# Kernel tuning notes

Hardware: AMD Instinct MI355X
Metric: run time of the kernel (lower is better)

## Reference

```python
import jax, jax.numpy as jnp
import numpy as np

QMAX = 255.0  # bit=8 unsigned activation range


def ste_round(x):
    # straight-through round: exact integer rounding in fwd, identity grad
    return x + jax.lax.stop_gradient(jnp.round(x) - x)


def conv3x3(x, w, stride=1):
    return jax.lax.conv_general_dilated(
        x, w, window_strides=(stride, stride), padding=((1, 1), (1, 1)),
        dimension_numbers=('NCHW', 'OIHW', 'NCHW'))


def setup_inputs() -> dict:
    key = jax.random.key(0)
    k0, k1, k2 = jax.random.split(key, 3)
    N, C, H, W = 64, 256, 28, 28
    # uint8 activations and int8 (symmetric) weights, stored as integer-valued fp32
    x = jax.random.randint(k0, (N, C, H, W), 0, 256).astype(jnp.float32)
    w1 = jax.random.randint(k1, (C, C, 3, 3), -128, 128).astype(jnp.float32)
    w2 = jax.random.randint(k2, (C, C, 3, 3), -128, 128).astype(jnp.float32)
    f = jnp.float32
    return dict(
        x=x, w1=w1, w2=w2,
        s_x=f(0.05), z_x=f(128.0),
        s_w1=f(0.01), s_conv1=f(0.08), z_conv1=f(120.0),
        s_w2=f(0.01), s_conv2=f(0.07), z_conv2=f(130.0),
        s_add=f(0.09), z_add=f(125.0))


def qconv(x_q, w_q, s_in, z_in, s_w, s_out, z_out, stride=1):
    # integer-arithmetic conv: sum((x - z_in) * w) then requantize
    acc = conv3x3(x_q - z_in, w_q, stride)
    M = s_in * s_w / s_out  # per-cluster requant multiplier (cluster 0)
    return jnp.clip(ste_round(M * acc) + z_out, 0.0, QMAX)


def qadd(a, s_a, z_a, b, s_b, z_b, s_out, z_out):
    # fused dequant of both branches + residual add + requant
    y = (s_a / s_out) * (a - z_a) + (s_b / s_out) * (b - z_b)
    return jnp.clip(ste_round(y) + z_out, 0.0, QMAX)


def reference(x, w1, w2, s_x, z_x, s_w1, s_conv1, z_conv1,
              s_w2, s_conv2, z_conv2, s_add, z_add):
    out = qconv(x, w1, s_x, z_x, s_w1, s_conv1, z_conv1)          # conv1
    out = qconv(out, w2, s_conv1, z_conv1, s_w2, s_conv2, z_conv2)  # conv2
    return qadd(x, s_x, z_x, out, s_conv2, z_conv2, s_add, z_add)   # shortcut
```

## Files before the change

kernel.cpp:

```cpp
#include <hip/hip_runtime.h>
#include <stdint.h>

#define HWP 784
#define NPOS 50176

typedef int int4v  __attribute__((ext_vector_type(4)));
typedef int int16v __attribute__((ext_vector_type(16)));
using as1_cv = const __attribute__((address_space(1))) void;
using as3_v  = __attribute__((address_space(3))) void;

__global__ __launch_bounds__(256) void k_x_to_nhwc(const float* __restrict__ x,
                                                   int8_t* __restrict__ x8) {
    __shared__ __align__(16) int8_t tile[64][116];
    int b = blockIdx.x;
    int ct = b & 3;
    int hwt = (b >> 2) % 7;
    int n = b / 28;
    int c0 = ct * 64, hw0 = hwt * 112;
    int tid = threadIdx.x;
#pragma unroll
    for (int k = 0; k < 28; ++k) {
        int e = tid + k * 256;
        int c = e / 112, hh = e % 112;
        float v = x[((size_t)(n * 256 + c0 + c)) * HWP + hw0 + hh];
        tile[c][hh] = (int8_t)((int)v - 128);
    }
    __syncthreads();
    int cc = tid & 63;
    int pb = tid >> 6;
#pragma unroll
    for (int j = 0; j < 28; ++j) {
        int pi = pb + j * 4;
        x8[((size_t)(n * HWP + hw0 + pi)) * 256 + c0 + cc] = tile[cc][pi];
    }
}

__global__ __launch_bounds__(256) void k_w_prep(const float* __restrict__ w,
                                                int8_t* __restrict__ w8,
                                                int* __restrict__ wsum) {
    __shared__ int red[256];
    const int oc = blockIdx.x;
    const int t = threadIdx.x;
    const float* src = w + (size_t)oc * 2304 + (size_t)t * 9;
    const int g = oc >> 5;
    const int l = ((t >> 4) & 1) * 32 + (oc & 31);
    const int j = t & 15;
    const int s2 = (t >> 5) & 1;
    const int kb = t >> 6;
    int acc = 0;
#pragma unroll
    for (int tap = 0; tap < 9; ++tap) {
        int wv = (int)src[tap];
        acc += wv;
        int oo = ((((tap * 4 + kb) * 2 + s2) * 8 + g) * 64 + l) * 16 + j;
        w8[oo] = (int8_t)wv;
    }
    red[t] = acc;
    __syncthreads();
    for (int st = 128; st > 0; st >>= 1) {
        if (t < st) red[t] += red[t + st];
        __syncthreads();
    }
    if (t == 0) wsum[oc] = red[0];
}

__global__ __launch_bounds__(256) void k_qconv(const int8_t* __restrict__ in8,
        const int8_t* __restrict__ w8, const int* __restrict__ wsum,
        const float* __restrict__ s_in_p, const float* __restrict__ s_w_p,
        const float* __restrict__ s_out_p, const float* __restrict__ z_in_p,
        const float* __restrict__ z_out_p, int8_t* __restrict__ out8) {
    __shared__ __align__(16) int8_t slab[32768];
    const int tid = threadIdx.x;
    const int lane = tid & 63;
    const int half = lane >> 5;
    const int wv = tid >> 6;
    const int p0 = blockIdx.x * 64;

    {
        const int base_byte = (p0 - 29) * 256;
        const int maxb = NPOS * 256 - 16;
#pragma unroll
        for (int i = 0; i < 8; ++i) {
            int chunkid = tid + i * 256;
            int q = chunkid >> 4;
            int cslot = chunkid & 15;
            int gchunk = cslot ^ (q & 15);
            int src = base_byte + q * 256 + gchunk * 16;
            src = src < 0 ? 0 : (src > maxb ? maxb : src);
            __builtin_amdgcn_global_load_lds((as1_cv*)(in8 + src),
                                             (as3_v*)&slab[chunkid * 16], 16, 0, 0);
        }
    }

    int rowpos[2], ph[2], pw[2];
#pragma unroll
    for (int mt = 0; mt < 2; ++mt) {
        rowpos[mt] = mt * 32 + (lane & 31);
        int p = p0 + rowpos[mt];
        int hw = p % HWP;
        ph[mt] = hw / 28;
        pw[mt] = hw % 28;
    }

    const int zi = (int)z_in_p[0] - 128;
    const int spl = (zi & 0xff) * 0x01010101;
    int4v pad;
    pad[0] = spl; pad[1] = spl; pad[2] = spl; pad[3] = spl;

    int16v acc[2][2];
#pragma unroll
    for (int mt = 0; mt < 2; ++mt)
#pragma unroll
        for (int nt = 0; nt < 2; ++nt)
#pragma unroll
            for (int r = 0; r < 16; ++r) acc[mt][nt][r] = 0;

    const int8_t* wlane = w8 + ((size_t)(wv * 2 * 64 + lane)) * 16;

    __syncthreads();

#pragma unroll 1
    for (int kb = 0; kb < 4; ++kb) {
#pragma unroll
        for (int tap = 0; tap < 9; ++tap) {
            const int dh = tap / 3 - 1;
            const int dw = tap % 3 - 1;
            const int8_t* wb = wlane + (size_t)(tap * 4 + kb) * 16384;
            int4v b0[2], b1[2];
#pragma unroll
            for (int nt = 0; nt < 2; ++nt) {
                b0[nt] = *(const int4v*)(wb + nt * 1024);
                b1[nt] = *(const int4v*)(wb + 8192 + nt * 1024);
            }
            int4v a0[2], a1[2];
#pragma unroll
            for (int mt = 0; mt < 2; ++mt) {
                int q = rowpos[mt] + dh * 28 + dw + 29;
                int sw = q & 15;
                int base = q * 256;
                int4v v0 = *(const int4v*)&slab[base + ((kb * 4 + half) ^ sw) * 16];
                int4v v1 = *(const int4v*)&slab[base + ((kb * 4 + 2 + half) ^ sw) * 16];
                bool ok = ((unsigned)(ph[mt] + dh) < 28u) & ((unsigned)(pw[mt] + dw) < 28u);
                a0[mt] = ok ? v0 : pad;
                a1[mt] = ok ? v1 : pad;
            }
#pragma unroll
            for (int mt = 0; mt < 2; ++mt)
#pragma unroll
                for (int nt = 0; nt < 2; ++nt) {
                    acc[mt][nt] = __builtin_amdgcn_mfma_i32_32x32x32_i8(a0[mt], b0[nt], acc[mt][nt], 0, 0, 0);
                    acc[mt][nt] = __builtin_amdgcn_mfma_i32_32x32x32_i8(a1[mt], b1[nt], acc[mt][nt], 0, 0, 0);
                }
        }
    }

    const float Mf = s_in_p[0] * s_w_p[0] / s_out_p[0];
    const float zof = z_out_p[0];
    const int zoffi = 128 - (int)z_in_p[0];
#pragma unroll
    for (int nt = 0; nt < 2; ++nt) {
        int oc = wv * 64 + nt * 32 + (lane & 31);
        int corr = zoffi * wsum[oc];
#pragma unroll
        for (int mt = 0; mt < 2; ++mt) {
#pragma unroll
            for (int r = 0; r < 16; ++r) {
                int row = (r & 3) + 8 * (r >> 2) + 4 * half;
                int pos = p0 + mt * 32 + row;
                float q = rintf(Mf * (float)(acc[mt][nt][r] + corr)) + zof;
                q = fminf(fmaxf(q, 0.0f), 255.0f);
                out8[(size_t)pos * 256 + oc] = (int8_t)((int)q - 128);
            }
        }
    }
}

__global__ __launch_bounds__(256) void k_final(const int8_t* __restrict__ x8,
        const int8_t* __restrict__ o2,
        const float* __restrict__ sxp, const float* __restrict__ zxp,
        const float* __restrict__ s2p, const float* __restrict__ z2p,
        const float* __restrict__ sap, const float* __restrict__ zap,
        float* __restrict__ out) {
    __shared__ __align__(16) int8_t ta[128 * 260 + 16];
    __shared__ __align__(16) int8_t tb[128 * 260 + 16];
    const int tid = threadIdx.x;
    const int p0 = blockIdx.x * 128;
    const uint32_t* xa = (const uint32_t*)(x8 + (size_t)p0 * 256);
    const uint32_t* xb = (const uint32_t*)(o2 + (size_t)p0 * 256);
    uint32_t* la = (uint32_t*)ta;
    uint32_t* lb = (uint32_t*)tb;
#pragma unroll
    for (int k = 0; k < 32; ++k) {
        int d = tid + k * 256;
        int idx = (d >> 6) * 65 + (d & 63);
        la[idx] = xa[d];
        lb[idx] = xb[d];
    }
    __syncthreads();
    const float ra = sxp[0] / sap[0];
    const float rb = s2p[0] / sap[0];
    const float zx = zxp[0];
    const float z2 = z2p[0];
    const float za = zap[0];
#pragma unroll 4
    for (int it = 0; it < 128; ++it) {
        int idx = tid + it * 256;
        int oc = idx >> 7;
        int pp = idx & 127;
        float av = (float)((int)ta[pp * 260 + oc] + 128) - zx;
        float bv = (float)((int)tb[pp * 260 + oc] + 128) - z2;
        float y = ra * av + rb * bv;
        float q = rintf(y) + za;
        q = fminf(fmaxf(q, 0.0f), 255.0f);
        int pz = p0 + pp;
        int n = pz / HWP, hh = pz % HWP;
        out[((size_t)(n * 256 + oc)) * HWP + hh] = q;
    }
}

extern "C" void kernel_launch(void* const* d_in, const int* in_sizes, int n_in,
                              void* d_out, int out_size, void* d_ws, size_t ws_size,
                              hipStream_t stream) {
    (void)in_sizes; (void)n_in; (void)out_size; (void)ws_size;
    const float* x    = (const float*)d_in[0];
    const float* w1   = (const float*)d_in[1];
    const float* w2   = (const float*)d_in[2];
    const float* s_x  = (const float*)d_in[3];
    const float* z_x  = (const float*)d_in[4];
    const float* s_w1 = (const float*)d_in[5];
    const float* s_c1 = (const float*)d_in[6];
    const float* z_c1 = (const float*)d_in[7];
    const float* s_w2 = (const float*)d_in[8];
    const float* s_c2 = (const float*)d_in[9];
    const float* z_c2 = (const float*)d_in[10];
    const float* s_ad = (const float*)d_in[11];
    const float* z_ad = (const float*)d_in[12];
    float* out = (float*)d_out;

    int8_t* ws   = (int8_t*)d_ws;
    int8_t* x8   = ws;
    int8_t* o1   = ws + 12845056;
    int8_t* o2   = ws + 25690112;
    int8_t* w8a  = ws + 38535168;
    int8_t* w8b  = ws + 39124992;
    int*    wsum1 = (int*)(ws + 39714816);
    int*    wsum2 = (int*)(ws + 39715840);

    k_x_to_nhwc<<<1792, 256, 0, stream>>>(x, x8);
    k_w_prep<<<256, 256, 0, stream>>>(w1, w8a, wsum1);
    k_w_prep<<<256, 256, 0, stream>>>(w2, w8b, wsum2);
    k_qconv<<<784, 256, 0, stream>>>(x8, w8a, wsum1, s_x, s_w1, s_c1, z_x, z_c1, o1);
    k_qconv<<<784, 256, 0, stream>>>(o1, w8b, wsum2, s_c1, s_w2, s_c2, z_c1, z_c2, o2);
    k_final<<<392, 256, 0, stream>>>(x8, o2, s_x, z_x, s_c2, z_c2, s_ad, z_ad, out);
}
```

Before: 225.5 us.

## Fuse residual add into conv2 and retile conv over positions and channel groups

The conv kernel now gives each block 256 positions and one 64-channel output group (grid 196x4) rather than 64 positions and all channels, so the input slab (now 80KB of LDS) is reused by every wave. Weight fragments are register double-buffered one step ahead, and the loop is reordered tap-outer so boundary masks are computed once per tap. The second conv is templated to fuse the quantized residual add and the NCHW float store, removing the separate final kernel and the o2 round trip through memory. In exchange, the larger LDS footprint reduces occupancy, and each input slab is loaded four times, once per channel-group block.

```diff
diff --git a/kernel.cpp b/kernel.cpp
--- a/kernel.cpp
+++ b/kernel.cpp
@@ -64,23 +64,28 @@
     if (t == 0) wsum[oc] = red[0];
 }
 
-__global__ __launch_bounds__(256) void k_qconv(const int8_t* __restrict__ in8,
+template<bool FUSED>
+__global__ __launch_bounds__(256) void k_qconv_t(const int8_t* __restrict__ in8,
         const int8_t* __restrict__ w8, const int* __restrict__ wsum,
         const float* __restrict__ s_in_p, const float* __restrict__ s_w_p,
         const float* __restrict__ s_out_p, const float* __restrict__ z_in_p,
-        const float* __restrict__ z_out_p, int8_t* __restrict__ out8) {
-    __shared__ __align__(16) int8_t slab[32768];
+        const float* __restrict__ z_out_p, int8_t* __restrict__ out8,
+        const int8_t* __restrict__ x8, const float* __restrict__ sxp,
+        const float* __restrict__ zxp, const float* __restrict__ sap,
+        const float* __restrict__ zap, float* __restrict__ outf) {
+    __shared__ __align__(16) int8_t slab[81920];
     const int tid = threadIdx.x;
     const int lane = tid & 63;
     const int half = lane >> 5;
     const int wv = tid >> 6;
-    const int p0 = blockIdx.x * 64;
+    const int p0 = blockIdx.x * 256;
+    const int g = blockIdx.y;
 
     {
         const int base_byte = (p0 - 29) * 256;
         const int maxb = NPOS * 256 - 16;
 #pragma unroll
-        for (int i = 0; i < 8; ++i) {
+        for (int i = 0; i < 20; ++i) {
             int chunkid = tid + i * 256;
             int q = chunkid >> 4;
             int cslot = chunkid & 15;
@@ -95,7 +100,7 @@
     int rowpos[2], ph[2], pw[2];
 #pragma unroll
     for (int mt = 0; mt < 2; ++mt) {
-        rowpos[mt] = mt * 32 + (lane & 31);
+        rowpos[mt] = wv * 64 + mt * 32 + (lane & 31);
         int p = p0 + rowpos[mt];
         int hw = p % HWP;
         ph[mt] = hw / 28;
@@ -115,106 +120,120 @@
 #pragma unroll
             for (int r = 0; r < 16; ++r) acc[mt][nt][r] = 0;
 
-    const int8_t* wlane = w8 + ((size_t)(wv * 2 * 64 + lane)) * 16;
+    const int8_t* wlane = w8 + g * 2048 + lane * 16;
+    auto loadB = [&](int u, int4v* b0, int4v* b1) {
+        const int8_t* wb = wlane + (size_t)u * 16384;
+        b0[0] = *(const int4v*)(wb);
+        b0[1] = *(const int4v*)(wb + 1024);
+        b1[0] = *(const int4v*)(wb + 8192);
+        b1[1] = *(const int4v*)(wb + 9216);
+    };
+
+    int4v cb0[2], cb1[2];
+    loadB(0, cb0, cb1);
 
     __syncthreads();
 
 #pragma unroll 1
-    for (int kb = 0; kb < 4; ++kb) {
-#pragma unroll
-        for (int tap = 0; tap < 9; ++tap) {
-            const int dh = tap / 3 - 1;
-            const int dw = tap % 3 - 1;
-            const int8_t* wb = wlane + (size_t)(tap * 4 + kb) * 16384;
-            int4v b0[2], b1[2];
-#pragma unroll
-            for (int nt = 0; nt < 2; ++nt) {
-                b0[nt] = *(const int4v*)(wb + nt * 1024);
-                b1[nt] = *(const int4v*)(wb + 8192 + nt * 1024);
-            }
+    for (int tap = 0; tap < 9; ++tap) {
+        const int dh = tap / 3 - 1;
+        const int dw = tap % 3 - 1;
+        int qbase[2];
+        bool okm[2];
+#pragma unroll
+        for (int mt = 0; mt < 2; ++mt) {
+            qbase[mt] = rowpos[mt] + dh * 28 + dw + 29;
+            okm[mt] = ((unsigned)(ph[mt] + dh) < 28u) & ((unsigned)(pw[mt] + dw) < 28u);
+        }
+#pragma unroll
+        for (int kb = 0; kb < 4; ++kb) {
+            const int u = tap * 4 + kb;
+            int4v nb0[2], nb1[2];
+            int un = u < 35 ? u + 1 : 35;
+            loadB(un, nb0, nb1);
             int4v a0[2], a1[2];
 #pragma unroll
             for (int mt = 0; mt < 2; ++mt) {
-                int q = rowpos[mt] + dh * 28 + dw + 29;
+                int q = qbase[mt];
                 int sw = q & 15;
                 int base = q * 256;
                 int4v v0 = *(const int4v*)&slab[base + ((kb * 4 + half) ^ sw) * 16];
                 int4v v1 = *(const int4v*)&slab[base + ((kb * 4 + 2 + half) ^ sw) * 16];
-                bool ok = ((unsigned)(ph[mt] + dh) < 28u) & ((unsigned)(pw[mt] + dw) < 28u);
-                a0[mt] = ok ? v0 : pad;
-                a1[mt] = ok ? v1 : pad;
+                a0[mt] = okm[mt] ? v0 : pad;
+                a1[mt] = okm[mt] ? v1 : pad;
             }
 #pragma unroll
             for (int mt = 0; mt < 2; ++mt)
 #pragma unroll
                 for (int nt = 0; nt < 2; ++nt) {
-                    acc[mt][nt] = __builtin_amdgcn_mfma_i32_32x32x32_i8(a0[mt], b0[nt], acc[mt][nt], 0, 0, 0);
-                    acc[mt][nt] = __builtin_amdgcn_mfma_i32_32x32x32_i8(a1[mt], b1[nt], acc[mt][nt], 0, 0, 0);
+                    acc[mt][nt] = __builtin_amdgcn_mfma_i32_32x32x32_i8(a0[mt], cb0[nt], acc[mt][nt], 0, 0, 0);
+                    acc[mt][nt] = __builtin_amdgcn_mfma_i32_32x32x32_i8(a1[mt], cb1[nt], acc[mt][nt], 0, 0, 0);
                 }
+#pragma unroll
+            for (int nt = 0; nt < 2; ++nt) { cb0[nt] = nb0[nt]; cb1[nt] = nb1[nt]; }
         }
     }
 
     const float Mf = s_in_p[0] * s_w_p[0] / s_out_p[0];
     const float zof = z_out_p[0];
     const int zoffi = 128 - (int)z_in_p[0];
-#pragma unroll
-    for (int nt = 0; nt < 2; ++nt) {
-        int oc = wv * 64 + nt * 32 + (lane & 31);
-        int corr = zoffi * wsum[oc];
-#pragma unroll
-        for (int mt = 0; mt < 2; ++mt) {
-#pragma unroll
-            for (int r = 0; r < 16; ++r) {
-                int row = (r & 3) + 8 * (r >> 2) + 4 * half;
-                int pos = p0 + mt * 32 + row;
-                float q = rintf(Mf * (float)(acc[mt][nt][r] + corr)) + zof;
-                q = fminf(fmaxf(q, 0.0f), 255.0f);
-                out8[(size_t)pos * 256 + oc] = (int8_t)((int)q - 128);
+
+    if (!FUSED) {
+#pragma unroll
+        for (int nt = 0; nt < 2; ++nt) {
+            int oc = g * 64 + nt * 32 + (lane & 31);
+            int corr = zoffi * wsum[oc];
+#pragma unroll
+            for (int mt = 0; mt < 2; ++mt) {
+#pragma unroll
+                for (int r = 0; r < 16; ++r) {
+                    int row = (r & 3) + 8 * (r >> 2) + 4 * half;
+                    int pos = p0 + wv * 64 + mt * 32 + row;
+                    float q = rintf(Mf * (float)(acc[mt][nt][r] + corr)) + zof;
+                    q = fminf(fmaxf(q, 0.0f), 255.0f);
+                    out8[(size_t)pos * 256 + oc] = (int8_t)((int)q - 128);
+                }
             }
         }
-    }
-}
-
-__global__ __launch_bounds__(256) void k_final(const int8_t* __restrict__ x8,
-        const int8_t* __restrict__ o2,
-        const float* __restrict__ sxp, const float* __restrict__ zxp,
-        const float* __restrict__ s2p, const float* __restrict__ z2p,
-        const float* __restrict__ sap, const float* __restrict__ zap,
-        float* __restrict__ out) {
-    __shared__ __align__(16) int8_t ta[128 * 260 + 16];
-    __shared__ __align__(16) int8_t tb[128 * 260 + 16];
-    const int tid = threadIdx.x;
-    const int p0 = blockIdx.x * 128;
-    const uint32_t* xa = (const uint32_t*)(x8 + (size_t)p0 * 256);
-    const uint32_t* xb = (const uint32_t*)(o2 + (size_t)p0 * 256);
-    uint32_t* la = (uint32_t*)ta;
-    uint32_t* lb = (uint32_t*)tb;
-#pragma unroll
-    for (int k = 0; k < 32; ++k) {
-        int d = tid + k * 256;
-        int idx = (d >> 6) * 65 + (d & 63);
-        la[idx] = xa[d];
-        lb[idx] = xb[d];
-    }
-    __syncthreads();
-    const float ra = sxp[0] / sap[0];
-    const float rb = s2p[0] / sap[0];
-    const float zx = zxp[0];
-    const float z2 = z2p[0];
-    const float za = zap[0];
-#pragma unroll 4
-    for (int it = 0; it < 128; ++it) {
-        int idx = tid + it * 256;
-        int oc = idx >> 7;
-        int pp = idx & 127;
-        float av = (float)((int)ta[pp * 260 + oc] + 128) - zx;
-        float bv = (float)((int)tb[pp * 260 + oc] + 128) - z2;
-        float y = ra * av + rb * bv;
-        float q = rintf(y) + za;
-        q = fminf(fmaxf(q, 0.0f), 255.0f);
-        int pz = p0 + pp;
-        int n = pz / HWP, hh = pz % HWP;
-        out[((size_t)(n * 256 + oc)) * HWP + hh] = q;
+    } else {
+        const float ra = sxp[0] / sap[0];
+        const float rb = s_out_p[0] / sap[0];
+        const float zx = zxp[0];
+        const float z2 = z_out_p[0];
+        const float za = zap[0];
+        __syncthreads();
+        float* tp = (float*)(slab + wv * 16640);
+#pragma unroll
+        for (int nt = 0; nt < 2; ++nt) {
+            int ocl = nt * 32 + (lane & 31);
+            int oc = g * 64 + ocl;
+            int corr = zoffi * wsum[oc];
+#pragma unroll
+            for (int mt = 0; mt < 2; ++mt) {
+#pragma unroll
+                for (int r = 0; r < 16; ++r) {
+                    int row = (r & 3) + 8 * (r >> 2) + 4 * half;
+                    int pl = mt * 32 + row;
+                    int pos = p0 + wv * 64 + pl;
+                    float q2 = rintf(Mf * (float)(acc[mt][nt][r] + corr)) + zof;
+                    q2 = fminf(fmaxf(q2, 0.0f), 255.0f);
+                    float av = (float)((int)x8[(size_t)pos * 256 + oc] + 128) - zx;
+                    float bv = q2 - z2;
+                    float y = ra * av + rb * bv;
+                    float qf = rintf(y) + za;
+                    qf = fminf(fmaxf(qf, 0.0f), 255.0f);
+                    tp[pl * 65 + ocl] = qf;
+                }
+            }
+        }
+        int p = p0 + wv * 64 + lane;
+        int n = p / HWP;
+        int hw = p % HWP;
+        float* obase = outf + (size_t)n * (256 * HWP) + hw + (size_t)(g * 64) * HWP;
+#pragma unroll 8
+        for (int oc = 0; oc < 64; ++oc) {
+            obase[(size_t)oc * HWP] = tp[lane * 65 + oc];
+        }
     }
 }
 
@@ -240,16 +259,18 @@
     int8_t* ws   = (int8_t*)d_ws;
     int8_t* x8   = ws;
     int8_t* o1   = ws + 12845056;
-    int8_t* o2   = ws + 25690112;
-    int8_t* w8a  = ws + 38535168;
-    int8_t* w8b  = ws + 39124992;
-    int*    wsum1 = (int*)(ws + 39714816);
-    int*    wsum2 = (int*)(ws + 39715840);
+    int8_t* w8a  = ws + 25690112;
+    int8_t* w8b  = ws + 26279936;
+    int*    wsum1 = (int*)(ws + 26869760);
+    int*    wsum2 = (int*)(ws + 26870784);
 
     k_x_to_nhwc<<<1792, 256, 0, stream>>>(x, x8);
     k_w_prep<<<256, 256, 0, stream>>>(w1, w8a, wsum1);
     k_w_prep<<<256, 256, 0, stream>>>(w2, w8b, wsum2);
-    k_qconv<<<784, 256, 0, stream>>>(x8, w8a, wsum1, s_x, s_w1, s_c1, z_x, z_c1, o1);
-    k_qconv<<<784, 256, 0, stream>>>(o1, w8b, wsum2, s_c1, s_w2, s_c2, z_c1, z_c2, o2);
-    k_final<<<392, 256, 0, stream>>>(x8, o2, s_x, z_x, s_c2, z_c2, s_ad, z_ad, out);
-}
+    k_qconv_t<false><<<dim3(196, 4), 256, 0, stream>>>(x8, w8a, wsum1,
+        s_x, s_w1, s_c1, z_x, z_c1, o1,
+        nullptr, nullptr, nullptr, nullptr, nullptr, nullptr);
+    k_qconv_t<true><<<dim3(196, 4), 256, 0, stream>>>(o1, w8b, wsum2,
+        s_c1, s_w2, s_c2, z_c1, z_c2, nullptr,
+        x8, s_x, z_x, s_ad, z_ad, out);
+}
```

Result: faster. 216.9 us (-3.8%).
